# Performance work log

Hardware: AMD Instinct MI355X
Metric: run time of the kernel (lower is better)

## Reference

```python
import math
import jax, jax.numpy as jnp
import numpy as np

B, S, D = 8, 2048, 512
D_MODEL = 512

def setup_inputs() -> dict:
    key = jax.random.key(0)
    kq, kk, kv = jax.random.split(key, 3)
    return {
        "query": jax.random.normal(kq, (B, S, D), dtype=jnp.float32),
        "key":   jax.random.normal(kk, (B, S, D), dtype=jnp.float32),
        "value": jax.random.normal(kv, (B, S, D), dtype=jnp.float32),
    }

def reference(query, key, value):
    # scores: [B, S, S]
    scores = jnp.einsum("bqd,bkd->bqk", query, key) / math.sqrt(D_MODEL)
    k = max(1, int(scores.shape[-1] * 0.1))
    top_scores, top_idx = jax.lax.top_k(scores, k)  # [B, S, k]
    # scatter top-k scores into a zero matrix (non-topk entries stay 0,
    # and DO participate in the softmax, matching the torch code)
    b_idx = jnp.arange(scores.shape[0])[:, None, None]
    q_idx = jnp.arange(scores.shape[1])[None, :, None]
    sparse = jnp.zeros_like(scores).at[b_idx, q_idx, top_idx].set(top_scores)
    attn = jax.nn.softmax(sparse, axis=-1)
    return jnp.einsum("bqk,bkd->bqd", attn, value)
```

## Files before the change

### kernel.cpp

```cpp
#include <hip/hip_runtime.h>
#include <math.h>

#define B_ 8
#define S_ 2048
#define D_ 512
#define KTOP 204
#define QK_SCALE 0.044194173824159216f

typedef short bfrag8 __attribute__((ext_vector_type(8)));
typedef float facc16 __attribute__((ext_vector_type(16)));

__device__ __forceinline__ unsigned short f2bf(float f) {
  unsigned u = __float_as_uint(f);
  u += 0x7FFFu + ((u >> 16) & 1);
  return (unsigned short)(u >> 16);
}

__device__ __forceinline__ unsigned fkey(float f) {
  unsigned b = __float_as_uint(f);
  return (b & 0x80000000u) ? ~b : (b | 0x80000000u);
}
__device__ __forceinline__ float keyfloat(unsigned k) {
  unsigned b = (k & 0x80000000u) ? (k & 0x7FFFFFFFu) : ~k;
  return __uint_as_float(b);
}

__device__ __forceinline__ void load16(const unsigned short* g, unsigned short* l) {
  __builtin_amdgcn_global_load_lds(
      (const __attribute__((address_space(1))) void*)g,
      (__attribute__((address_space(3))) void*)l, 16, 0, 0);
}

__global__ __launch_bounds__(256) void cvt_qk(const float* __restrict__ Q,
                                              const float* __restrict__ K,
                                              unsigned short* __restrict__ Qb,
                                              unsigned short* __restrict__ Kb) {
  const float* in = blockIdx.y ? K : Q;
  unsigned short* out = blockIdx.y ? Kb : Qb;
  int i = (blockIdx.x * 256 + threadIdx.x) * 4;
  float4 v = *(const float4*)(in + i);
  ushort4 o;
  o.x = f2bf(v.x); o.y = f2bf(v.y); o.z = f2bf(v.z); o.w = f2bf(v.w);
  *(ushort4*)(out + i) = o;
}

__global__ __launch_bounds__(256) void transpose_v(const float* __restrict__ V,
                                                   unsigned short* __restrict__ VT) {
  __shared__ float tile[32][33];
  int b = blockIdx.z;
  int d0 = blockIdx.x * 32, k0 = blockIdx.y * 32;
  const float* Vb = V + (size_t)b * S_ * D_;
  unsigned short* VTb = VT + (size_t)b * D_ * S_;
  int c = threadIdx.x & 31, r = threadIdx.x >> 5;
#pragma unroll
  for (int rr = 0; rr < 32; rr += 8)
    tile[r + rr][c] = Vb[(size_t)(k0 + r + rr) * D_ + d0 + c];
  __syncthreads();
#pragma unroll
  for (int rr = 0; rr < 32; rr += 8)
    VTb[(size_t)(d0 + r + rr) * S_ + k0 + c] = f2bf(tile[c][r + rr]);
}


__device__ __forceinline__ void stage64(const unsigned short* M, int ld, int k0,
                                        int tid, unsigned short* dst) {
  const int wave = tid >> 6;
  const int row = tid >> 3;
  const int col = ((tid & 7) ^ (row & 7)) * 8;
  unsigned short* wdst = dst + wave * 512;
  const unsigned short* src = M + (size_t)row * ld + k0 + col;
#pragma unroll
  for (int s = 0; s < 4; ++s)
    load16(src + (size_t)(s * 32) * ld, wdst + s * 2048);
}

__device__ __forceinline__ void mfma_step64(const unsigned short* sA, const unsigned short* sB,
                                            int mrow, int nrow, int lane,
                                            facc16 (&acc)[2][2]) {
  const int l31 = lane & 31, b5 = lane >> 5, l7 = lane & 7;
#pragma unroll
  for (int c = 0; c < 4; ++c) {
    const int slot = ((c * 2 + b5) ^ l7) * 8;
    bfrag8 af[2], bq[2];
#pragma unroll
    for (int i = 0; i < 2; ++i)
      af[i] = *(const bfrag8*)(sA + (mrow + 32 * i + l31) * 64 + slot);
#pragma unroll
    for (int j2 = 0; j2 < 2; ++j2)
      bq[j2] = *(const bfrag8*)(sB + (nrow + 32 * j2 + l31) * 64 + slot);
#pragma unroll
    for (int i = 0; i < 2; ++i)
#pragma unroll
      for (int j2 = 0; j2 < 2; ++j2)
        acc[i][j2] = __builtin_amdgcn_mfma_f32_32x32x16_bf16(af[i], bq[j2], acc[i][j2], 0, 0, 0);
  }
}

__global__ __launch_bounds__(256) void gemm_qk(
    const unsigned short* __restrict__ A, int lda, long long astr,
    const unsigned short* __restrict__ Bm, int ldb, long long bstr,
    float* __restrict__ C, int ldc, long long cstr,
    int kdim, float scale) {
  const unsigned j = blockIdx.x + 16u * blockIdx.y + 256u * blockIdx.z;
  const unsigned bz = j & 7u;
  const unsigned q = j >> 3;
  const unsigned by = q & 15u;
  const unsigned bx = q >> 4;

  __shared__ unsigned short smA[2][128 * 64];
  __shared__ unsigned short smB[2][128 * 64];
  const int tid = threadIdx.x;
  const int wave = tid >> 6, lane = tid & 63;
  const unsigned short* Ab = A + (long long)bz * astr + (size_t)(by * 128) * lda;
  const unsigned short* Bb = Bm + (long long)bz * bstr + (size_t)(bx * 128) * ldb;
  const int mrow = 64 * (wave >> 1);
  const int nrow = 64 * (wave & 1);

  facc16 acc[2][2];
#pragma unroll
  for (int i = 0; i < 2; ++i)
#pragma unroll
    for (int j2 = 0; j2 < 2; ++j2)
#pragma unroll
      for (int r = 0; r < 16; ++r) acc[i][j2][r] = 0.f;

  stage64(Ab, lda, 0, tid, smA[0]);
  stage64(Bb, ldb, 0, tid, smB[0]);
  __syncthreads();

  for (int k0 = 0; k0 < kdim; k0 += 128) {
    stage64(Ab, lda, k0 + 64, tid, smA[1]);
    stage64(Bb, ldb, k0 + 64, tid, smB[1]);
    mfma_step64(smA[0], smB[0], mrow, nrow, lane, acc);
    __syncthreads();
    if (k0 + 128 < kdim) {
      stage64(Ab, lda, k0 + 128, tid, smA[0]);
      stage64(Bb, ldb, k0 + 128, tid, smB[0]);
    }
    mfma_step64(smA[1], smB[1], mrow, nrow, lane, acc);
    __syncthreads();
  }

  float* Cb = C + (long long)bz * cstr;
  const int mg = by * 128 + mrow;
  const int ng = bx * 128 + nrow;
  const int l31 = lane & 31, b5 = lane >> 5;
#pragma unroll
  for (int i = 0; i < 2; ++i)
#pragma unroll
    for (int j2 = 0; j2 < 2; ++j2)
#pragma unroll
      for (int r = 0; r < 16; ++r) {
        const int row = mg + 32 * i + (r & 3) + 8 * (r >> 2) + 4 * b5;
        const int col = ng + 32 * j2 + l31;
        Cb[(size_t)row * ldc + col] = acc[i][j2][r] * scale;
      }
}

__global__ __launch_bounds__(256) void gemm_pv(
    const unsigned short* __restrict__ A, int lda, long long astr,
    const unsigned short* __restrict__ Bm, int ldb, long long bstr,
    float* __restrict__ C, int ldc, long long cstr,
    int kdim, float scale) {
  const unsigned j = blockIdx.x + 4u * blockIdx.y + 64u * blockIdx.z;
  const unsigned bz = j & 7u;
  const unsigned q = j >> 3;
  const unsigned bx = q & 3u;
  const unsigned by = q >> 2;

  __shared__ unsigned short smA[2][128 * 64];
  __shared__ unsigned short smB[2][128 * 64];
  const int tid = threadIdx.x;
  const int wave = tid >> 6, lane = tid & 63;
  const unsigned short* Ab = A + (long long)bz * astr + (size_t)(by * 128) * lda;
  const unsigned short* Bb = Bm + (long long)bz * bstr + (size_t)(bx * 128) * ldb;
  const int mrow = 64 * (wave >> 1);
  const int nrow = 64 * (wave & 1);

  facc16 acc[2][2];
#pragma unroll
  for (int i = 0; i < 2; ++i)
#pragma unroll
    for (int j2 = 0; j2 < 2; ++j2)
#pragma unroll
      for (int r = 0; r < 16; ++r) acc[i][j2][r] = 0.f;

  stage64(Ab, lda, 0, tid, smA[0]);
  stage64(Bb, ldb, 0, tid, smB[0]);
  __syncthreads();

  for (int k0 = 0; k0 < kdim; k0 += 128) {
    stage64(Ab, lda, k0 + 64, tid, smA[1]);
    stage64(Bb, ldb, k0 + 64, tid, smB[1]);
    mfma_step64(smA[0], smB[0], mrow, nrow, lane, acc);
    __syncthreads();
    if (k0 + 128 < kdim) {
      stage64(Ab, lda, k0 + 128, tid, smA[0]);
      stage64(Bb, ldb, k0 + 128, tid, smB[0]);
    }
    mfma_step64(smA[1], smB[1], mrow, nrow, lane, acc);
    __syncthreads();
  }

  float* Cb = C + (long long)bz * cstr;
  const int mg = by * 128 + mrow;
  const int ng = bx * 128 + nrow;
  const int l31 = lane & 31, b5 = lane >> 5;
#pragma unroll
  for (int i = 0; i < 2; ++i)
#pragma unroll
    for (int j2 = 0; j2 < 2; ++j2)
#pragma unroll
      for (int r = 0; r < 16; ++r) {
        const int row = mg + 32 * i + (r & 3) + 8 * (r >> 2) + 4 * b5;
        const int col = ng + 32 * j2 + l31;
        Cb[(size_t)row * ldc + col] = acc[i][j2][r] * scale;
      }
}

__device__ __forceinline__ unsigned sel256(const unsigned* bins, int lane,
                                           unsigned krem, unsigned* krem_out) {
  const uint4 b = *(const uint4*)(bins + lane * 4);
  const unsigned s = b.x + b.y + b.z + b.w;
  unsigned t = s;
#pragma unroll
  for (int off = 1; off < 64; off <<= 1) {
    unsigned u = (unsigned)__shfl_down((int)t, off);
    t += (lane + off < 64) ? u : 0u;
  }
  const unsigned texcl = t - s;
  const unsigned c3 = texcl + b.w;
  const unsigned c2 = c3 + b.z;
  const unsigned c1 = c2 + b.y;
  const unsigned c0 = c1 + b.x;
  unsigned pack = 0;
  if (c0 >= krem && c1 < krem)    pack = ((krem - c1) << 8) | (lane * 4 + 0);
  if (c1 >= krem && c2 < krem)    pack = ((krem - c2) << 8) | (lane * 4 + 1);
  if (c2 >= krem && c3 < krem)    pack = ((krem - c3) << 8) | (lane * 4 + 2);
  if (c3 >= krem && texcl < krem) pack = ((krem - texcl) << 8) | (lane * 4 + 3);
#pragma unroll
  for (int off = 1; off < 64; off <<= 1)
    pack |= (unsigned)__shfl_xor((int)pack, off);
  *krem_out = pack >> 8;
  return pack & 255u;
}

__global__ __launch_bounds__(256) void topk_softmax(float* __restrict__ scores) {
  __shared__ unsigned binsAll[4][256];
  const int tid = threadIdx.x;
  const int wave = tid >> 6, lane = tid & 63;
  const long long row = (long long)blockIdx.x * 4 + wave;
  float* srow = scores + row * 2048;
  unsigned* bins = binsAll[wave];

  unsigned k[32];
#pragma unroll
  for (int c = 0; c < 4; ++c) {
    float4 a = *(const float4*)(srow + c * 512 + lane * 8);
    float4 b = *(const float4*)(srow + c * 512 + lane * 8 + 4);
    k[c * 8 + 0] = fkey(a.x); k[c * 8 + 1] = fkey(a.y);
    k[c * 8 + 2] = fkey(a.z); k[c * 8 + 3] = fkey(a.w);
    k[c * 8 + 4] = fkey(b.x); k[c * 8 + 5] = fkey(b.y);
    k[c * 8 + 6] = fkey(b.z); k[c * 8 + 7] = fkey(b.w);
  }

  unsigned kmax = 0;
#pragma unroll
  for (int i = 0; i < 32; ++i) kmax = max(kmax, k[i]);
#pragma unroll
  for (int off = 1; off < 64; off <<= 1)
    kmax = max(kmax, (unsigned)__shfl_xor((int)kmax, off));
  const float m = fmaxf(keyfloat(kmax), 0.f);

  {
    uint4 z; z.x = 0; z.y = 0; z.z = 0; z.w = 0;
    *(uint4*)(bins + lane * 4) = z;
  }
#pragma unroll
  for (int i = 0; i < 32; ++i) {
    const int t = (int)(k[i] >> 16) - 0xBF00;
    if (t >= 1) atomicAdd(&bins[min(t, 255)], 1u);
  }
  unsigned krem;
  const unsigned d1 = sel256(bins, lane, KTOP, &krem);

  unsigned tkey;
  if (d1 >= 1u && d1 <= 254u) {
    const unsigned top16 = 0xBF00u + d1;
    { uint4 z; z.x = 0; z.y = 0; z.z = 0; z.w = 0; *(uint4*)(bins + lane * 4) = z; }
#pragma unroll
    for (int i = 0; i < 32; ++i)
      if ((k[i] >> 16) == top16) atomicAdd(&bins[(k[i] >> 8) & 255u], 1u);
    const unsigned b1 = sel256(bins, lane, krem, &krem);
    const unsigned top24 = (top16 << 8) | b1;
    { uint4 z; z.x = 0; z.y = 0; z.z = 0; z.w = 0; *(uint4*)(bins + lane * 4) = z; }
#pragma unroll
    for (int i = 0; i < 32; ++i)
      if ((k[i] >> 8) == top24) atomicAdd(&bins[k[i] & 255u], 1u);
    const unsigned b0 = sel256(bins, lane, krem, &krem);
    tkey = (top24 << 8) | b0;
  } else {
    krem = KTOP;
    unsigned prefix = 0, mmask = 0;
    for (int shift = 24; shift >= 0; shift -= 8) {
      { uint4 z; z.x = 0; z.y = 0; z.z = 0; z.w = 0; *(uint4*)(bins + lane * 4) = z; }
#pragma unroll
      for (int i = 0; i < 32; ++i)
        if ((k[i] & mmask) == prefix) atomicAdd(&bins[(k[i] >> shift) & 255u], 1u);
      const unsigned dig = sel256(bins, lane, krem, &krem);
      prefix |= dig << shift;
      mmask |= 0xFFu << shift;
    }
    tkey = prefix;
  }

  unsigned cut;
  {
    unsigned tiem = 0;
#pragma unroll
    for (int i = 0; i < 32; ++i)
      if (k[i] == tkey) tiem |= 1u << i;
    unsigned need = krem;
    for (;;) {
      unsigned myidx = 0xFFFFFFFFu;
      if (tiem) {
        int i = __ffs((int)tiem) - 1;
        myidx = ((unsigned)(i >> 3)) * 512u + (unsigned)lane * 8u + (unsigned)(i & 7);
      }
      unsigned minidx = myidx;
#pragma unroll
      for (int off = 1; off < 64; off <<= 1)
        minidx = min(minidx, (unsigned)__shfl_xor((int)minidx, off));
      if (--need == 0 || minidx == 0xFFFFFFFFu) { cut = minidx; break; }
      if (myidx == minidx) tiem &= tiem - 1;
    }
  }

  const float eqw = __expf(keyfloat(tkey) - m);
  const float base = __expf(-m);
  float zsum = 0.f;
#pragma unroll
  for (int i = 0; i < 32; ++i) {
    const unsigned key = k[i];
    const unsigned idx = ((unsigned)(i >> 3)) * 512u + (unsigned)lane * 8u + (unsigned)(i & 7);
    float w;
    if (key > tkey) w = __expf(keyfloat(key) - m);
    else w = (key == tkey && idx <= cut) ? eqw : base;
    zsum += w;
    k[i] = __float_as_uint(w);
  }
#pragma unroll
  for (int off = 1; off < 64; off <<= 1) zsum += __shfl_xor(zsum, off);
  const float invZ = 1.f / zsum;

  unsigned short* arow = (unsigned short*)scores + row * 4096;
#pragma unroll
  for (int c = 0; c < 4; ++c) {
    union { unsigned short u[8]; int4 v4; } pk;
#pragma unroll
    for (int j = 0; j < 8; ++j)
      pk.u[j] = f2bf(__uint_as_float(k[c * 8 + j]) * invZ);
    *(int4*)(arow + c * 512 + lane * 8) = pk.v4;
  }
}

extern "C" void kernel_launch(void* const* d_in, const int* in_sizes, int n_in,
                              void* d_out, int out_size, void* d_ws, size_t ws_size,
                              hipStream_t stream) {
  const float* Q = (const float*)d_in[0];
  const float* K = (const float*)d_in[1];
  const float* V = (const float*)d_in[2];
  float* out = (float*)d_out;
  char* ws = (char*)d_ws;
  unsigned short* Qb = (unsigned short*)(ws);
  unsigned short* Kb = (unsigned short*)(ws + ((size_t)16 << 20));
  unsigned short* VT = (unsigned short*)(ws + ((size_t)32 << 20));
  float* scores = (float*)(ws + ((size_t)48 << 20));

  const int nel = B_ * S_ * D_;
  cvt_qk<<<dim3(nel / 1024, 2), 256, 0, stream>>>(Q, K, Qb, Kb);
  transpose_v<<<dim3(D_ / 32, S_ / 32, B_), 256, 0, stream>>>(V, VT);
  gemm_qk<<<dim3(S_ / 128, S_ / 128, B_), 256, 0, stream>>>(
      Qb, D_, (long long)S_ * D_, Kb, D_, (long long)S_ * D_,
      scores, S_, (long long)S_ * S_, D_, QK_SCALE);
  topk_softmax<<<B_ * S_ / 4, 256, 0, stream>>>(scores);
  gemm_pv<<<dim3(D_ / 128, S_ / 128, B_), 256, 0, stream>>>(
      (const unsigned short*)scores, 4096, (long long)S_ * 4096,
      VT, S_, (long long)D_ * S_, out, D_, (long long)S_ * D_, S_, 1.0f);
}
```

Before: 273.2 us.

## Split each top-k softmax row across two cooperating waves

```diff
diff --git a/kernel.cpp b/kernel.cpp
--- a/kernel.cpp
+++ b/kernel.cpp
@@ -246,16 +246,19 @@
 }
 
 __global__ __launch_bounds__(256) void topk_softmax(float* __restrict__ scores) {
-  __shared__ unsigned binsAll[4][256];
+  __shared__ unsigned binsAll[2][256];
+  __shared__ unsigned xchg[2][4];
   const int tid = threadIdx.x;
   const int wave = tid >> 6, lane = tid & 63;
-  const long long row = (long long)blockIdx.x * 4 + wave;
-  float* srow = scores + row * 2048;
-  unsigned* bins = binsAll[wave];
-
-  unsigned k[32];
-#pragma unroll
-  for (int c = 0; c < 4; ++c) {
+  const int pair = wave >> 1, h = wave & 1;
+  const long long row = (long long)blockIdx.x * 2 + pair;
+  float* srow = scores + row * 2048 + h * 1024;
+  unsigned* bins = binsAll[pair];
+  unsigned* xch = xchg[pair];
+
+  unsigned k[16];
+#pragma unroll
+  for (int c = 0; c < 2; ++c) {
     float4 a = *(const float4*)(srow + c * 512 + lane * 8);
     float4 b = *(const float4*)(srow + c * 512 + lane * 8 + 4);
     k[c * 8 + 0] = fkey(a.x); k[c * 8 + 1] = fkey(a.y);
@@ -264,85 +267,114 @@
     k[c * 8 + 6] = fkey(b.z); k[c * 8 + 7] = fkey(b.w);
   }
 
+  {
+    uint2 z; z.x = 0; z.y = 0;
+    *(uint2*)(bins + (h * 64 + lane) * 2) = z;
+  }
   unsigned kmax = 0;
 #pragma unroll
-  for (int i = 0; i < 32; ++i) kmax = max(kmax, k[i]);
+  for (int i = 0; i < 16; ++i) kmax = max(kmax, k[i]);
 #pragma unroll
   for (int off = 1; off < 64; off <<= 1)
     kmax = max(kmax, (unsigned)__shfl_xor((int)kmax, off));
+  if (lane == 0) xch[h] = kmax;
+  __syncthreads();
+  kmax = max(xch[0], xch[1]);
   const float m = fmaxf(keyfloat(kmax), 0.f);
 
-  {
-    uint4 z; z.x = 0; z.y = 0; z.z = 0; z.w = 0;
-    *(uint4*)(bins + lane * 4) = z;
-  }
-#pragma unroll
-  for (int i = 0; i < 32; ++i) {
+#pragma unroll
+  for (int i = 0; i < 16; ++i) {
     const int t = (int)(k[i] >> 16) - 0xBF00;
     if (t >= 1) atomicAdd(&bins[min(t, 255)], 1u);
   }
-  unsigned krem;
-  const unsigned d1 = sel256(bins, lane, KTOP, &krem);
-
-  unsigned tkey;
-  if (d1 >= 1u && d1 <= 254u) {
-    const unsigned top16 = 0xBF00u + d1;
-    { uint4 z; z.x = 0; z.y = 0; z.z = 0; z.w = 0; *(uint4*)(bins + lane * 4) = z; }
-#pragma unroll
-    for (int i = 0; i < 32; ++i)
-      if ((k[i] >> 16) == top16) atomicAdd(&bins[(k[i] >> 8) & 255u], 1u);
-    const unsigned b1 = sel256(bins, lane, krem, &krem);
-    const unsigned top24 = (top16 << 8) | b1;
-    { uint4 z; z.x = 0; z.y = 0; z.z = 0; z.w = 0; *(uint4*)(bins + lane * 4) = z; }
-#pragma unroll
-    for (int i = 0; i < 32; ++i)
-      if ((k[i] >> 8) == top24) atomicAdd(&bins[k[i] & 255u], 1u);
-    const unsigned b0 = sel256(bins, lane, krem, &krem);
-    tkey = (top24 << 8) | b0;
-  } else {
-    krem = KTOP;
-    unsigned prefix = 0, mmask = 0;
-    for (int shift = 24; shift >= 0; shift -= 8) {
-      { uint4 z; z.x = 0; z.y = 0; z.z = 0; z.w = 0; *(uint4*)(bins + lane * 4) = z; }
-#pragma unroll
-      for (int i = 0; i < 32; ++i)
+  __syncthreads();
+  if (h == 0) {
+    unsigned kr;
+    const unsigned d = sel256(bins, lane, KTOP, &kr);
+    if (lane == 0) xch[2] = (kr << 8) | d;
+    asm volatile("s_waitcnt lgkmcnt(0)" ::: "memory");
+    uint4 z4; z4.x = 0; z4.y = 0; z4.z = 0; z4.w = 0;
+    *(uint4*)(bins + lane * 4) = z4;
+  }
+  __syncthreads();
+  unsigned pack = xch[2];
+  const unsigned d1 = pack & 255u;
+  unsigned krem = pack >> 8;
+
+  const bool fb = (d1 < 1u || d1 > 254u);
+  unsigned prefix, mmask;
+  if (!fb) { prefix = (0xBF00u + d1) << 16; mmask = 0xFFFF0000u; }
+  else     { prefix = 0u; mmask = 0u; krem = KTOP; }
+
+  for (int s = 1; s <= 4; ++s) {
+    const bool active = fb || (s <= 2);
+    const int shift = fb ? (32 - 8 * s) : ((s == 1) ? 8 : 0);
+    if (active) {
+#pragma unroll
+      for (int i = 0; i < 16; ++i)
         if ((k[i] & mmask) == prefix) atomicAdd(&bins[(k[i] >> shift) & 255u], 1u);
-      const unsigned dig = sel256(bins, lane, krem, &krem);
-      prefix |= dig << shift;
+    }
+    __syncthreads();
+    if (h == 0 && active) {
+      unsigned kr;
+      const unsigned d = sel256(bins, lane, krem, &kr);
+      if (lane == 0) xch[2] = (kr << 8) | d;
+      asm volatile("s_waitcnt lgkmcnt(0)" ::: "memory");
+      uint4 z4; z4.x = 0; z4.y = 0; z4.z = 0; z4.w = 0;
+      *(uint4*)(bins + lane * 4) = z4;
+    }
+    __syncthreads();
+    if (active) {
+      pack = xch[2];
+      prefix |= (pack & 255u) << shift;
+      krem = pack >> 8;
       mmask |= 0xFFu << shift;
     }
-    tkey = prefix;
-  }
-
-  unsigned cut;
-  {
-    unsigned tiem = 0;
-#pragma unroll
-    for (int i = 0; i < 32; ++i)
-      if (k[i] == tkey) tiem |= 1u << i;
-    unsigned need = krem;
+  }
+  const unsigned tkey = prefix;
+
+  unsigned tiem = 0;
+#pragma unroll
+  for (int i = 0; i < 16; ++i)
+    if (k[i] == tkey) tiem |= 1u << i;
+  unsigned tc = (unsigned)__popc(tiem);
+#pragma unroll
+  for (int off = 1; off < 64; off <<= 1)
+    tc += (unsigned)__shfl_xor((int)tc, off);
+  if (h == 0 && lane == 0) xch[3] = tc;
+  __syncthreads();
+  const unsigned tcA = xch[3];
+  const int whichHalf = (krem <= tcA) ? 0 : 1;
+  if (h == whichHalf) {
+    unsigned need = whichHalf ? (krem - tcA) : krem;
+    unsigned cutl;
     for (;;) {
       unsigned myidx = 0xFFFFFFFFu;
       if (tiem) {
         int i = __ffs((int)tiem) - 1;
-        myidx = ((unsigned)(i >> 3)) * 512u + (unsigned)lane * 8u + (unsigned)(i & 7);
+        myidx = (unsigned)(h * 1024) + ((unsigned)(i >> 3)) * 512u +
+                (unsigned)lane * 8u + (unsigned)(i & 7);
       }
       unsigned minidx = myidx;
 #pragma unroll
       for (int off = 1; off < 64; off <<= 1)
         minidx = min(minidx, (unsigned)__shfl_xor((int)minidx, off));
-      if (--need == 0 || minidx == 0xFFFFFFFFu) { cut = minidx; break; }
+      if (--need == 0 || minidx == 0xFFFFFFFFu) { cutl = minidx; break; }
       if (myidx == minidx) tiem &= tiem - 1;
     }
-  }
+    if (lane == 0) xch[2] = cutl;
+  }
+  __syncthreads();
+  const unsigned cut = xch[2];
 
   const float eqw = __expf(keyfloat(tkey) - m);
   const float base = __expf(-m);
   float zsum = 0.f;
 #pragma unroll
-  for (int i = 0; i < 32; ++i) {
+  for (int i = 0; i < 16; ++i) {
     const unsigned key = k[i];
-    const unsigned idx = ((unsigned)(i >> 3)) * 512u + (unsigned)lane * 8u + (unsigned)(i & 7);
+    const unsigned idx = (unsigned)(h * 1024) + ((unsigned)(i >> 3)) * 512u +
+                         (unsigned)lane * 8u + (unsigned)(i & 7);
     float w;
     if (key > tkey) w = __expf(keyfloat(key) - m);
     else w = (key == tkey && idx <= cut) ? eqw : base;
@@ -351,11 +383,14 @@
   }
 #pragma unroll
   for (int off = 1; off < 64; off <<= 1) zsum += __shfl_xor(zsum, off);
-  const float invZ = 1.f / zsum;
-
-  unsigned short* arow = (unsigned short*)scores + row * 4096;
-#pragma unroll
-  for (int c = 0; c < 4; ++c) {
+  if (lane == 0) xch[h] = __float_as_uint(zsum);
+  __syncthreads();
+  const float Z = __uint_as_float(xch[0]) + __uint_as_float(xch[1]);
+  const float invZ = 1.f / Z;
+
+  unsigned short* arow = (unsigned short*)scores + row * 4096 + h * 1024;
+#pragma unroll
+  for (int c = 0; c < 2; ++c) {
     union { unsigned short u[8]; int4 v4; } pk;
 #pragma unroll
     for (int j = 0; j < 8; ++j)
@@ -383,7 +418,7 @@
   gemm_qk<<<dim3(S_ / 128, S_ / 128, B_), 256, 0, stream>>>(
       Qb, D_, (long long)S_ * D_, Kb, D_, (long long)S_ * D_,
       scores, S_, (long long)S_ * S_, D_, QK_SCALE);
-  topk_softmax<<<B_ * S_ / 4, 256, 0, stream>>>(scores);
+  topk_softmax<<<B_ * S_ / 2, 256, 0, stream>>>(scores);
   gemm_pv<<<dim3(D_ / 128, S_ / 128, B_), 256, 0, stream>>>(
       (const unsigned short*)scores, 4096, (long long)S_ * 4096,
       VT, S_, (long long)D_ * S_, out, D_, (long long)S_ * D_, S_, 1.0f);
```

Result: slower. 282.6 us (+3.4%).
